# Kernel tuning notes

Hardware: AMD Instinct MI355X
Metric: run time of the kernel (lower is better)

Reference implementation:

```python
import jax, jax.numpy as jnp
import numpy as np

B, S, L, C, H, D, CP = 32, 4, 64, 32, 4, 8, 16  # batch, tracks, bins, c_msa, heads, d_head, c_pair


def _ln(x, g, b, eps=1e-5):
    m = jnp.mean(x, axis=-1, keepdims=True)
    v = jnp.mean((x - m) ** 2, axis=-1, keepdims=True)
    return (x - m) / jnp.sqrt(v + eps) * g + b


def setup_inputs() -> dict:
    key = jax.random.key(0)
    ks = jax.random.split(key, 20)
    n = lambda k, shape, s=0.1: jax.random.normal(k, shape, jnp.float32) * s
    return dict(
        chip_ctcf=n(ks[0], (B, L), 1.0),
        chip_hac=n(ks[1], (B, L), 1.0),
        chip_me1=n(ks[2], (B, L), 1.0),
        chip_me3=n(ks[3], (B, L), 1.0),
        bulk_map=n(ks[4], (B, 1, L, L), 1.0),
        we_w=n(ks[5], (C, 1)), we_b=jnp.zeros((C,), jnp.float32),
        pos=n(ks[6], (1, 1, L, C)),
        mn_g=jnp.ones((C,), jnp.float32), mn_b=jnp.zeros((C,), jnp.float32),
        wq=n(ks[7], (C, C)), bq=jnp.zeros((C,), jnp.float32),
        wk=n(ks[8], (C, C)), bk=jnp.zeros((C,), jnp.float32),
        wv=n(ks[9], (C, C)), bv=jnp.zeros((C,), jnp.float32),
        wo=n(ks[10], (C, C)), bo=jnp.zeros((C,), jnp.float32),
        an_g=jnp.ones((C,), jnp.float32), an_b=jnp.zeros((C,), jnp.float32),
        conv_w=n(ks[11], (H,)), conv_b=jnp.zeros((H,), jnp.float32),
        gate_w=n(ks[12], (H, D, D)), gate_b=jnp.zeros((H, D), jnp.float32),
        pp_w=n(ks[13], (CP, C * C), 0.03), pp_b=jnp.zeros((CP,), jnp.float32),
        ada_g=jnp.ones((CP,), jnp.float32), ada_b=jnp.zeros((CP,), jnp.float32),
        ada_alpha=jnp.ones((1,), jnp.float32),
    )


def reference(chip_ctcf, chip_hac, chip_me1, chip_me3, bulk_map,
              we_w, we_b, pos, mn_g, mn_b,
              wq, bq, wk, bk, wv, bv, wo, bo, an_g, an_b,
              conv_w, conv_b, gate_w, gate_b,
              pp_w, pp_b, ada_g, ada_b, ada_alpha):
    # 1) build MSA: (B, S=4, L, C)
    signals = jnp.stack([chip_ctcf, chip_hac, chip_me1, chip_me3], axis=1)  # (B,S,L)
    msa = signals[..., None] * we_w[:, 0] + we_b                            # Linear(1,C)
    x = _ln(msa + pos, mn_g, mn_b)                                          # (B,S,L,C)

    # 2) row self-attention with bulk-derived per-head bias
    q = (x @ wq.T + bq).reshape(B, S, L, H, D)
    k = (x @ wk.T + bk).reshape(B, S, L, H, D)
    v = (x @ wv.T + bv).reshape(B, S, L, H, D)
    scores = jnp.einsum('bslhd,bsmhd->bshlm', q, k) / jnp.sqrt(jnp.float32(D))
    bias = bulk_map * conv_w.reshape(1, H, 1, 1) + conv_b.reshape(1, H, 1, 1)  # 1x1 conv -> (B,H,L,L)
    attn = jax.nn.softmax(scores + bias[:, None], axis=-1)                     # (B,S,H,L,L)
    out = jnp.einsum('bshlm,bsmhd->bshld', attn, v)
    gate = jax.nn.sigmoid(jnp.einsum('hcd,bshld->bshlc', gate_w, out)
                          + gate_b[None, None, :, None, :])
    out = out * gate
    out = out.transpose(0, 1, 3, 2, 4).reshape(B, S, L, C)
    out = out @ wo.T + bo
    x = _ln(x + out, an_g, an_b)                                            # post-attn LayerNorm

    # 3) outer-product (of max over tracks) pair features
    m = jnp.max(x, axis=1)                                                  # (B,L,C)
    pair = jnp.einsum('bic,bjd->bijcd', m, m).reshape(B, L, L, C * C)       # (B,L,L,1024)
    nrm = jnp.sqrt(jnp.sum(pair * pair, axis=-1, keepdims=True))
    pair = pair / jnp.maximum(nrm, 1e-6)                                    # F.normalize
    feat = pair @ pp_w.T + pp_b                                             # (B,L,L,CP)
    feat = feat + ada_alpha * _ln(feat, ada_g, ada_b)                       # AdaNorm
    feat = jax.nn.silu(feat)
    return feat.transpose(0, 3, 1, 2)                                       # (B,CP,L,L)
```

## Files before the change

### kernel.cpp

```cpp
#include <hip/hip_runtime.h>
#include <hip/hip_bf16.h>

#define NB 32
#define NS 4
#define NL 64
#define NC 32
#define NH 4
#define ND 8
#define NCP 16

using fp = const float* __restrict__;

__global__ __launch_bounds__(256) void k1_attn(
    fp ctcf, fp hac, fp me1, fp me3, fp bulk,
    fp we_w, fp we_b, fp pos, fp mn_g, fp mn_b,
    fp wq, fp bq, fp wk, fp bk, fp wv, fp bv,
    fp wo, fp bo, fp an_g, fp an_b,
    fp conv_w, fp conv_b, fp gate_w, fp gate_b,
    float* __restrict__ xpostT)
{
    __shared__ float ks_s[NC*NL];
    __shared__ float vs_s[NC*NL];
    __shared__ float ao_s[NC*NL];
    __shared__ float bulk_s[NL*65];
    __shared__ float red1[256], red2[256];

    const int t = threadIdx.x;
    const int w = t >> 6;
    const int l = t & 63;
    const int b = blockIdx.x >> 2;
    const int s = blockIdx.x & 3;

    for (int idx = t; idx < NL*NL; idx += 256)
        bulk_s[(idx >> 6)*65 + (idx & 63)] = bulk[b*NL*NL + idx];

    fp sigp = (s == 0) ? ctcf : (s == 1) ? hac : (s == 2) ? me1 : me3;
    const float sig = sigp[b*NL + l];

    float x[NC];
    float mean = 0.f;
#pragma unroll
    for (int c = 0; c < NC; c++){
        x[c] = sig * we_w[c] + we_b[c] + pos[l*NC + c];
        mean += x[c];
    }
    mean *= (1.f/NC);
    float var = 0.f;
#pragma unroll
    for (int c = 0; c < NC; c++){ float d = x[c] - mean; var += d*d; }
    var *= (1.f/NC);
    float inv = rsqrtf(var + 1e-5f);
#pragma unroll
    for (int c = 0; c < NC; c++) x[c] = (x[c] - mean)*inv*mn_g[c] + mn_b[c];

    float q[ND];
#pragma unroll
    for (int e8 = 0; e8 < ND; e8++){
        int e = w*ND + e8;
        float aq = bq[e], ak = bk[e], av = bv[e];
#pragma unroll
        for (int c = 0; c < NC; c++){
            float xv = x[c];
            aq += xv * wq[e*NC + c];
            ak += xv * wk[e*NC + c];
            av += xv * wv[e*NC + c];
        }
        q[e8] = aq;
        ks_s[e*NL + l] = ak;
        vs_s[e*NL + l] = av;
    }
    __syncthreads();

    const float rs8 = 0.35355339059327373f;
    const float cw = conv_w[w], cb = conv_b[w];
    float srow[NL];
    float mx = -1e30f;
    for (int m = 0; m < NL; m++){
        float dot = 0.f;
#pragma unroll
        for (int d = 0; d < ND; d++)
            dot += q[d] * ks_s[(w*ND + d)*NL + m];
        float v = dot*rs8 + bulk_s[l*65 + m]*cw + cb;
        srow[m] = v;
        mx = fmaxf(mx, v);
    }
    float sm = 0.f;
    for (int m = 0; m < NL; m++){ srow[m] = __expf(srow[m] - mx); sm += srow[m]; }
    float is = 1.f / sm;
    float o[ND];
#pragma unroll
    for (int d = 0; d < ND; d++) o[d] = 0.f;
    for (int m = 0; m < NL; m++){
        float a = srow[m] * is;
#pragma unroll
        for (int d = 0; d < ND; d++)
            o[d] += a * vs_s[(w*ND + d)*NL + m];
    }
#pragma unroll
    for (int c8 = 0; c8 < ND; c8++){
        float g = gate_b[w*ND + c8];
#pragma unroll
        for (int d = 0; d < ND; d++) g += gate_w[(w*ND + c8)*ND + d] * o[d];
        ao_s[(w*ND + c8)*NL + l] = o[c8] * (1.f/(1.f + __expf(-g)));
    }
    __syncthreads();

    float p8[ND];
    float psum = 0.f, psq = 0.f;
#pragma unroll
    for (int c8 = 0; c8 < ND; c8++){
        int c = w*ND + c8;
        float a = bo[c];
#pragma unroll
        for (int e = 0; e < NC; e++) a += ao_s[e*NL + l] * wo[c*NC + e];
        float val = x[c] + a;
        p8[c8] = val; psum += val; psq += val*val;
    }
    red1[w*64 + l] = psum;
    red2[w*64 + l] = psq;
    __syncthreads();
    float sum = 0.f, ssq = 0.f;
#pragma unroll
    for (int ww = 0; ww < 4; ww++){ sum += red1[ww*64 + l]; ssq += red2[ww*64 + l]; }
    mean = sum * (1.f/NC);
    var  = ssq * (1.f/NC) - mean*mean;
    inv  = rsqrtf(var + 1e-5f);
#pragma unroll
    for (int c8 = 0; c8 < ND; c8++){
        int c = w*ND + c8;
        xpostT[((b*NS + s)*NC + c)*NL + l] = (p8[c8] - mean)*inv*an_g[c] + an_b[c];
    }
}

__global__ __launch_bounds__(256) void k23_pair(
    const float* __restrict__ xpostT, fp pp_w,
    fp pp_b, fp ada_g, fp ada_b, fp ada_alpha,
    float* __restrict__ out)
{
    __shared__ float ppws[8*NC*NC];
    __shared__ float mh[NC*NL];
    __shared__ float u[NCP*4*NC];

    const int b  = blockIdx.x >> 4;
    const int it = blockIdx.x & 15;
    const int t  = threadIdx.x;
    const int w  = t >> 6;
    const int j  = t & 63;

    const float* xb = xpostT + b*NS*NC*NL;
#pragma unroll
    for (int k = 0; k < 8; k++){
        int cj = k*256 + t;
        float v = xb[cj];
        v = fmaxf(v, xb[NC*NL + cj]);
        v = fmaxf(v, xb[2*NC*NL + cj]);
        v = fmaxf(v, xb[3*NC*NL + cj]);
        mh[cj] = v;
    }
    __syncthreads();

    if (t < NL){
        float sq = 0.f;
#pragma unroll
        for (int c = 0; c < NC; c++){ float v = mh[c*NL + t]; sq += v*v; }
        u[t] = 1.f / fmaxf(sqrtf(sq), 1e-3f);
    }
    {
        const float4* src = (const float4*)(pp_w);
        float4* dst = (float4*)ppws;
#pragma unroll
        for (int k = 0; k < 8; k++) dst[k*256 + t] = src[k*256 + t];
    }
    __syncthreads();

#pragma unroll
    for (int k = 0; k < 8; k++){
        int cj = k*256 + t;
        mh[cj] *= u[cj & 63];
    }
    __syncthreads();

    float md[NC];
#pragma unroll
    for (int c = 0; c < NC; c++) md[c] = mh[c*NL + j];

#pragma unroll
    for (int loop = 0; loop < 4; loop++){
        int idx = loop*256 + t;
        int d  = idx & 31;
        int ip = (idx >> 5) & 3;
        int pl = idx >> 7;
        int i  = it*4 + ip;
        float acc = 0.f;
#pragma unroll
        for (int c = 0; c < NC; c++)
            acc += mh[c*NL + i] * ppws[pl*1024 + c*32 + d];
        u[pl*128 + ip*32 + d] = acc;
    }
    __syncthreads();

    {
        const float4* src = (const float4*)(pp_w + 8*NC*NC);
        float4* dst = (float4*)ppws;
#pragma unroll
        for (int k = 0; k < 8; k++) dst[k*256 + t] = src[k*256 + t];
    }
    __syncthreads();

#pragma unroll
    for (int loop = 0; loop < 4; loop++){
        int idx = loop*256 + t;
        int d  = idx & 31;
        int ip = (idx >> 5) & 3;
        int pl = idx >> 7;
        int i  = it*4 + ip;
        float acc = 0.f;
#pragma unroll
        for (int c = 0; c < NC; c++)
            acc += mh[c*NL + i] * ppws[pl*1024 + c*32 + d];
        u[(8 + pl)*128 + ip*32 + d] = acc;
    }
    __syncthreads();

    float f[NCP];
#pragma unroll 1
    for (int p = 0; p < NCP; p++){
        float a = 0.f;
#pragma unroll
        for (int d = 0; d < NC; d++)
            a += u[p*128 + w*32 + d] * md[d];
        f[p] = a;
    }

    const float alpha = ada_alpha[0];
    float fsum = 0.f, fsq = 0.f;
#pragma unroll
    for (int p = 0; p < NCP; p++){
        float v = f[p] + pp_b[p];
        f[p] = v; fsum += v; fsq += v*v;
    }
    float fmean = fsum * (1.f/NCP);
    float fvar  = fsq * (1.f/NCP) - fmean*fmean;
    float finv  = rsqrtf(fvar + 1e-5f);
    const int i = it*4 + w;
#pragma unroll
    for (int p = 0; p < NCP; p++){
        float v = f[p] + alpha * ((f[p] - fmean)*finv*ada_g[p] + ada_b[p]);
        out[((b*NCP + p)*NL + i)*NL + j] = v / (1.f + __expf(-v));
    }
}

extern "C" void kernel_launch(void* const* d_in, const int* in_sizes, int n_in,
                              void* d_out, int out_size, void* d_ws, size_t ws_size,
                              hipStream_t stream)
{
    float* xpostT = (float*)d_ws;

    k1_attn<<<NB*NS, 256, 0, stream>>>(
        (fp)d_in[0], (fp)d_in[1], (fp)d_in[2], (fp)d_in[3], (fp)d_in[4],
        (fp)d_in[5], (fp)d_in[6], (fp)d_in[7], (fp)d_in[8], (fp)d_in[9],
        (fp)d_in[10], (fp)d_in[11], (fp)d_in[12], (fp)d_in[13], (fp)d_in[14], (fp)d_in[15],
        (fp)d_in[16], (fp)d_in[17], (fp)d_in[18], (fp)d_in[19],
        (fp)d_in[20], (fp)d_in[21], (fp)d_in[22], (fp)d_in[23], xpostT);

    k23_pair<<<NB*16, 256, 0, stream>>>(
        xpostT, (fp)d_in[24], (fp)d_in[25], (fp)d_in[26], (fp)d_in[27], (fp)d_in[28],
        (float*)d_out);
}
```

Before: 143.0 us.

## Split attention kernel into two row-halves with key-split softmax across lane pairs

The attention kernel now launches two blocks per (batch, track), each handling 32 query rows. Within a block, each query row is processed by a pair of lanes, each covering half of the keys, and the max, sum and output are combined with xor shuffles. The intent is to double the grid from 128 to 256 blocks so more of the GPU's compute units are busy, and to shrink each thread's score array to cut register pressure. In exchange, each block recomputes the full Q/K/V projection and LayerNorm for all 64 rows, and the code adds shared-memory staging plus an extra reduction step for the post-attention LayerNorm.

Result: no change. 142.8 us (median of 2 runs) (-0.2%).

```diff
diff --git a/kernel.cpp b/kernel.cpp
--- a/kernel.cpp
+++ b/kernel.cpp
@@ -19,20 +19,27 @@
     fp conv_w, fp conv_b, fp gate_w, fp gate_b,
     float* __restrict__ xpostT)
 {
+    __shared__ float qs_s[NC*NL];
     __shared__ float ks_s[NC*NL];
     __shared__ float vs_s[NC*NL];
+    __shared__ float xs_s[NC*NL];
     __shared__ float ao_s[NC*NL];
-    __shared__ float bulk_s[NL*65];
-    __shared__ float red1[256], red2[256];
-
-    const int t = threadIdx.x;
-    const int w = t >> 6;
-    const int l = t & 63;
-    const int b = blockIdx.x >> 2;
-    const int s = blockIdx.x & 3;
-
-    for (int idx = t; idx < NL*NL; idx += 256)
-        bulk_s[(idx >> 6)*65 + (idx & 63)] = bulk[b*NL*NL + idx];
+    __shared__ float bulk_s[32*65];
+    __shared__ float red1[32*8], red2[32*8];
+    __shared__ float mstat[32], istat[32];
+
+    const int t    = threadIdx.x;
+    const int w    = t >> 6;
+    const int l    = t & 63;
+    const int bx   = blockIdx.x;
+    const int b    = bx >> 3;
+    const int s    = (bx >> 1) & 3;
+    const int half = bx & 1;
+
+    for (int idx = t; idx < 32*NL; idx += 256){
+        int lr = idx >> 6, m = idx & 63;
+        bulk_s[lr*65 + m] = bulk[b*NL*NL + (half*32 + lr)*NL + m];
+    }
 
     fp sigp = (s == 0) ? ctcf : (s == 1) ? hac : (s == 2) ? me1 : me3;
     const float sig = sigp[b*NL + l];
@@ -53,7 +60,6 @@
 #pragma unroll
     for (int c = 0; c < NC; c++) x[c] = (x[c] - mean)*inv*mn_g[c] + mn_b[c];
 
-    float q[ND];
 #pragma unroll
     for (int e8 = 0; e8 < ND; e8++){
         int e = w*ND + e8;
@@ -65,70 +71,98 @@
             ak += xv * wk[e*NC + c];
             av += xv * wv[e*NC + c];
         }
-        q[e8] = aq;
+        qs_s[e*NL + l] = aq;
         ks_s[e*NL + l] = ak;
         vs_s[e*NL + l] = av;
-    }
-    __syncthreads();
+        xs_s[e*NL + l] = x[e];
+    }
+    __syncthreads();
+
+    const int rl  = l >> 1;
+    const int r   = half*32 + rl;
+    const int mh_ = l & 1;
+    const int m0  = mh_*32;
+
+    float q8[ND];
+#pragma unroll
+    for (int d = 0; d < ND; d++) q8[d] = qs_s[(w*ND + d)*NL + r];
 
     const float rs8 = 0.35355339059327373f;
     const float cw = conv_w[w], cb = conv_b[w];
-    float srow[NL];
+    float srow[32];
     float mx = -1e30f;
-    for (int m = 0; m < NL; m++){
+    for (int mi = 0; mi < 32; mi++){
+        int m = m0 + mi;
         float dot = 0.f;
 #pragma unroll
         for (int d = 0; d < ND; d++)
-            dot += q[d] * ks_s[(w*ND + d)*NL + m];
-        float v = dot*rs8 + bulk_s[l*65 + m]*cw + cb;
-        srow[m] = v;
+            dot += q8[d] * ks_s[(w*ND + d)*NL + m];
+        float v = dot*rs8 + bulk_s[rl*65 + m]*cw + cb;
+        srow[mi] = v;
         mx = fmaxf(mx, v);
     }
+    mx = fmaxf(mx, __shfl_xor(mx, 1));
     float sm = 0.f;
-    for (int m = 0; m < NL; m++){ srow[m] = __expf(srow[m] - mx); sm += srow[m]; }
+    for (int mi = 0; mi < 32; mi++){ srow[mi] = __expf(srow[mi] - mx); sm += srow[mi]; }
+    sm += __shfl_xor(sm, 1);
     float is = 1.f / sm;
+
     float o[ND];
 #pragma unroll
     for (int d = 0; d < ND; d++) o[d] = 0.f;
-    for (int m = 0; m < NL; m++){
-        float a = srow[m] * is;
+    for (int mi = 0; mi < 32; mi++){
+        float a = srow[mi] * is;
 #pragma unroll
         for (int d = 0; d < ND; d++)
-            o[d] += a * vs_s[(w*ND + d)*NL + m];
-    }
-#pragma unroll
-    for (int c8 = 0; c8 < ND; c8++){
+            o[d] += a * vs_s[(w*ND + d)*NL + m0 + mi];
+    }
+#pragma unroll
+    for (int d = 0; d < ND; d++) o[d] += __shfl_xor(o[d], 1);
+
+#pragma unroll
+    for (int k = 0; k < 4; k++){
+        int c8 = mh_*4 + k;
         float g = gate_b[w*ND + c8];
 #pragma unroll
         for (int d = 0; d < ND; d++) g += gate_w[(w*ND + c8)*ND + d] * o[d];
-        ao_s[(w*ND + c8)*NL + l] = o[c8] * (1.f/(1.f + __expf(-g)));
-    }
-    __syncthreads();
-
-    float p8[ND];
+        ao_s[(w*ND + c8)*NL + r] = o[c8] * (1.f/(1.f + __expf(-g)));
+    }
+    __syncthreads();
+
+    const int r3  = t & 31;
+    const int rg  = half*32 + r3;
+    const int cg  = t >> 5;
+    float vals[4];
     float psum = 0.f, psq = 0.f;
 #pragma unroll
-    for (int c8 = 0; c8 < ND; c8++){
-        int c = w*ND + c8;
+    for (int k = 0; k < 4; k++){
+        int c = cg*4 + k;
         float a = bo[c];
 #pragma unroll
-        for (int e = 0; e < NC; e++) a += ao_s[e*NL + l] * wo[c*NC + e];
-        float val = x[c] + a;
-        p8[c8] = val; psum += val; psq += val*val;
-    }
-    red1[w*64 + l] = psum;
-    red2[w*64 + l] = psq;
-    __syncthreads();
-    float sum = 0.f, ssq = 0.f;
-#pragma unroll
-    for (int ww = 0; ww < 4; ww++){ sum += red1[ww*64 + l]; ssq += red2[ww*64 + l]; }
-    mean = sum * (1.f/NC);
-    var  = ssq * (1.f/NC) - mean*mean;
-    inv  = rsqrtf(var + 1e-5f);
-#pragma unroll
-    for (int c8 = 0; c8 < ND; c8++){
-        int c = w*ND + c8;
-        xpostT[((b*NS + s)*NC + c)*NL + l] = (p8[c8] - mean)*inv*an_g[c] + an_b[c];
+        for (int e = 0; e < NC; e++) a += ao_s[e*NL + rg] * wo[c*NC + e];
+        float val = xs_s[c*NL + rg] + a;
+        vals[k] = val; psum += val; psq += val*val;
+    }
+    red1[r3*8 + cg] = psum;
+    red2[r3*8 + cg] = psq;
+    __syncthreads();
+    if (t < 32){
+        float sum = 0.f, ssq = 0.f;
+#pragma unroll
+        for (int g = 0; g < 8; g++){ sum += red1[t*8 + g]; ssq += red2[t*8 + g]; }
+        float mn = sum * (1.f/NC);
+        float vr = ssq * (1.f/NC) - mn*mn;
+        mstat[t] = mn;
+        istat[t] = rsqrtf(vr + 1e-5f);
+    }
+    __syncthreads();
+    {
+        float mn = mstat[r3], iv = istat[r3];
+#pragma unroll
+        for (int k = 0; k < 4; k++){
+            int c = cg*4 + k;
+            xpostT[((b*NS + s)*NC + c)*NL + rg] = (vals[k] - mn)*iv*an_g[c] + an_b[c];
+        }
     }
 }
 
@@ -256,7 +290,7 @@
 {
     float* xpostT = (float*)d_ws;
 
-    k1_attn<<<NB*NS, 256, 0, stream>>>(
+    k1_attn<<<NB*NS*2, 256, 0, stream>>>(
         (fp)d_in[0], (fp)d_in[1], (fp)d_in[2], (fp)d_in[3], (fp)d_in[4],
         (fp)d_in[5], (fp)d_in[6], (fp)d_in[7], (fp)d_in[8], (fp)d_in[9],
         (fp)d_in[10], (fp)d_in[11], (fp)d_in[12], (fp)d_in[13], (fp)d_in[14], (fp)d_in[15],
```

## Fuse attention and pair-feature kernels into one kernel with recomputed attention

Applied to the files above, without the earlier changes.

Merges the two kernels into a single launch: each block handles one batch and an 8-row slab of output, and recomputes all four tracks' attention (one wave per track, each thread doing all heads) instead of reading a workspace tensor. This removes the intermediate global round-trip and a launch boundary, and swaps the padded bulk tile for an XOR-swizzled layout. In exchange, attention work is duplicated 8x across blocks, per-thread register pressure rises sharply (q[32], ao[32], x[32]), and the grid shrinks to 256 blocks.

Measured after the change: 247.8 us. 1.73x slower.

```diff
diff --git a/kernel.cpp b/kernel.cpp
--- a/kernel.cpp
+++ b/kernel.cpp
@@ -11,32 +11,34 @@
 
 using fp = const float* __restrict__;
 
-__global__ __launch_bounds__(256) void k1_attn(
+__global__ __launch_bounds__(256, 2) void kall(
     fp ctcf, fp hac, fp me1, fp me3, fp bulk,
     fp we_w, fp we_b, fp pos, fp mn_g, fp mn_b,
     fp wq, fp bq, fp wk, fp bk, fp wv, fp bv,
     fp wo, fp bo, fp an_g, fp an_b,
     fp conv_w, fp conv_b, fp gate_w, fp gate_b,
-    float* __restrict__ xpostT)
+    fp pp_w, fp pp_b, fp ada_g, fp ada_b, fp ada_alpha,
+    float* __restrict__ out)
 {
-    __shared__ float ks_s[NC*NL];
-    __shared__ float vs_s[NC*NL];
-    __shared__ float ao_s[NC*NL];
-    __shared__ float bulk_s[NL*65];
-    __shared__ float red1[256], red2[256];
-
-    const int t = threadIdx.x;
-    const int w = t >> 6;
-    const int l = t & 63;
-    const int b = blockIdx.x >> 2;
-    const int s = blockIdx.x & 3;
-
-    for (int idx = t; idx < NL*NL; idx += 256)
-        bulk_s[(idx >> 6)*65 + (idx & 63)] = bulk[b*NL*NL + idx];
-
-    fp sigp = (s == 0) ? ctcf : (s == 1) ? hac : (s == 2) ? me1 : me3;
+    __shared__ float A[8192];
+    __shared__ float V[8192];
+    __shared__ float bulk_s[4096];
+
+    const int t  = threadIdx.x;
+    const int w  = t >> 6;
+    const int l  = t & 63;
+    const int b  = blockIdx.x >> 3;
+    const int it = blockIdx.x & 7;
+
+#pragma unroll
+    for (int k = 0; k < 16; k++){
+        int idx = k*256 + t;
+        int row = idx >> 6, col = idx & 63;
+        bulk_s[row*64 + (col ^ (row & 31))] = bulk[b*4096 + idx];
+    }
+
+    fp sigp = (w == 0) ? ctcf : (w == 1) ? hac : (w == 2) ? me1 : me3;
     const float sig = sigp[b*NL + l];
-
     float x[NC];
     float mean = 0.f;
 #pragma unroll
@@ -53,10 +55,9 @@
 #pragma unroll
     for (int c = 0; c < NC; c++) x[c] = (x[c] - mean)*inv*mn_g[c] + mn_b[c];
 
-    float q[ND];
-#pragma unroll
-    for (int e8 = 0; e8 < ND; e8++){
-        int e = w*ND + e8;
+    float q[NC];
+#pragma unroll
+    for (int e = 0; e < NC; e++){
         float aq = bq[e], ak = bk[e], av = bv[e];
 #pragma unroll
         for (int c = 0; c < NC; c++){
@@ -65,109 +66,99 @@
             ak += xv * wk[e*NC + c];
             av += xv * wv[e*NC + c];
         }
-        q[e8] = aq;
-        ks_s[e*NL + l] = ak;
-        vs_s[e*NL + l] = av;
+        q[e] = aq;
+        A[w*2048 + e*64 + l] = ak;
+        V[w*2048 + e*64 + l] = av;
     }
     __syncthreads();
 
     const float rs8 = 0.35355339059327373f;
-    const float cw = conv_w[w], cb = conv_b[w];
-    float srow[NL];
-    float mx = -1e30f;
-    for (int m = 0; m < NL; m++){
-        float dot = 0.f;
-#pragma unroll
-        for (int d = 0; d < ND; d++)
-            dot += q[d] * ks_s[(w*ND + d)*NL + m];
-        float v = dot*rs8 + bulk_s[l*65 + m]*cw + cb;
-        srow[m] = v;
-        mx = fmaxf(mx, v);
-    }
-    float sm = 0.f;
-    for (int m = 0; m < NL; m++){ srow[m] = __expf(srow[m] - mx); sm += srow[m]; }
-    float is = 1.f / sm;
-    float o[ND];
-#pragma unroll
-    for (int d = 0; d < ND; d++) o[d] = 0.f;
-    for (int m = 0; m < NL; m++){
-        float a = srow[m] * is;
-#pragma unroll
-        for (int d = 0; d < ND; d++)
-            o[d] += a * vs_s[(w*ND + d)*NL + m];
-    }
-#pragma unroll
-    for (int c8 = 0; c8 < ND; c8++){
-        float g = gate_b[w*ND + c8];
-#pragma unroll
-        for (int d = 0; d < ND; d++) g += gate_w[(w*ND + c8)*ND + d] * o[d];
-        ao_s[(w*ND + c8)*NL + l] = o[c8] * (1.f/(1.f + __expf(-g)));
-    }
-    __syncthreads();
-
-    float p8[ND];
-    float psum = 0.f, psq = 0.f;
-#pragma unroll
-    for (int c8 = 0; c8 < ND; c8++){
-        int c = w*ND + c8;
-        float a = bo[c];
-#pragma unroll
-        for (int e = 0; e < NC; e++) a += ao_s[e*NL + l] * wo[c*NC + e];
-        float val = x[c] + a;
-        p8[c8] = val; psum += val; psq += val*val;
-    }
-    red1[w*64 + l] = psum;
-    red2[w*64 + l] = psq;
-    __syncthreads();
-    float sum = 0.f, ssq = 0.f;
-#pragma unroll
-    for (int ww = 0; ww < 4; ww++){ sum += red1[ww*64 + l]; ssq += red2[ww*64 + l]; }
-    mean = sum * (1.f/NC);
-    var  = ssq * (1.f/NC) - mean*mean;
-    inv  = rsqrtf(var + 1e-5f);
-#pragma unroll
-    for (int c8 = 0; c8 < ND; c8++){
-        int c = w*ND + c8;
-        xpostT[((b*NS + s)*NC + c)*NL + l] = (p8[c8] - mean)*inv*an_g[c] + an_b[c];
-    }
-}
-
-__global__ __launch_bounds__(256) void k23_pair(
-    const float* __restrict__ xpostT, fp pp_w,
-    fp pp_b, fp ada_g, fp ada_b, fp ada_alpha,
-    float* __restrict__ out)
-{
-    __shared__ float ppws[8*NC*NC];
-    __shared__ float mh[NC*NL];
-    __shared__ float u[NCP*4*NC];
-
-    const int b  = blockIdx.x >> 4;
-    const int it = blockIdx.x & 15;
-    const int t  = threadIdx.x;
-    const int w  = t >> 6;
-    const int j  = t & 63;
-
-    const float* xb = xpostT + b*NS*NC*NL;
-#pragma unroll
-    for (int k = 0; k < 8; k++){
-        int cj = k*256 + t;
-        float v = xb[cj];
-        v = fmaxf(v, xb[NC*NL + cj]);
-        v = fmaxf(v, xb[2*NC*NL + cj]);
-        v = fmaxf(v, xb[3*NC*NL + cj]);
-        mh[cj] = v;
-    }
-    __syncthreads();
-
+    float ao[NC];
+    for (int h = 0; h < NH; h++){
+        const float cw = conv_w[h], cb = conv_b[h];
+        float srow[NL];
+        float mx = -1e30f;
+        for (int m = 0; m < NL; m++){
+            float dot = 0.f;
+#pragma unroll
+            for (int d = 0; d < ND; d++)
+                dot += q[h*ND + d] * A[w*2048 + (h*ND + d)*64 + m];
+            float v = dot*rs8 + bulk_s[l*64 + (m ^ (l & 31))]*cw + cb;
+            srow[m] = v;
+            mx = fmaxf(mx, v);
+        }
+        float sm = 0.f;
+        for (int m = 0; m < NL; m++){ srow[m] = __expf(srow[m] - mx); sm += srow[m]; }
+        float is = 1.f / sm;
+        float o[ND];
+#pragma unroll
+        for (int d = 0; d < ND; d++) o[d] = 0.f;
+        for (int m = 0; m < NL; m++){
+            float a = srow[m] * is;
+#pragma unroll
+            for (int d = 0; d < ND; d++)
+                o[d] += a * V[w*2048 + (h*ND + d)*64 + m];
+        }
+#pragma unroll
+        for (int c8 = 0; c8 < ND; c8++){
+            float g = gate_b[h*ND + c8];
+#pragma unroll
+            for (int d = 0; d < ND; d++) g += gate_w[(h*ND + c8)*ND + d] * o[d];
+            ao[h*ND + c8] = o[c8] * (1.f/(1.f + __expf(-g)));
+        }
+    }
+    __syncthreads();
+
+    {
+        float xp[NC];
+        float mn2 = 0.f;
+#pragma unroll
+        for (int c = 0; c < NC; c++){
+            float a = bo[c];
+#pragma unroll
+            for (int e = 0; e < NC; e++) a += ao[e] * wo[c*NC + e];
+            float val = x[c] + a;
+            xp[c] = val; mn2 += val;
+        }
+        mn2 *= (1.f/NC);
+        float vr = 0.f;
+#pragma unroll
+        for (int c = 0; c < NC; c++){ float d = xp[c] - mn2; vr += d*d; }
+        vr *= (1.f/NC);
+        float iv = rsqrtf(vr + 1e-5f);
+#pragma unroll
+        for (int c = 0; c < NC; c++)
+            A[w*2048 + c*64 + l] = (xp[c] - mn2)*iv*an_g[c] + an_b[c];
+    }
+    __syncthreads();
+
+#pragma unroll
+    for (int k = 0; k < 8; k++){
+        int cl = k*256 + t;
+        float v = A[cl];
+        v = fmaxf(v, A[2048 + cl]);
+        v = fmaxf(v, A[4096 + cl]);
+        v = fmaxf(v, A[6144 + cl]);
+        V[cl] = v;
+    }
+    __syncthreads();
     if (t < NL){
         float sq = 0.f;
 #pragma unroll
-        for (int c = 0; c < NC; c++){ float v = mh[c*NL + t]; sq += v*v; }
-        u[t] = 1.f / fmaxf(sqrtf(sq), 1e-3f);
-    }
+        for (int c = 0; c < NC; c++){ float v = V[c*64 + t]; sq += v*v; }
+        V[6144 + t] = 1.f / fmaxf(sqrtf(sq), 1e-3f);
+    }
+    __syncthreads();
+#pragma unroll
+    for (int k = 0; k < 8; k++){
+        int cl = k*256 + t;
+        V[cl] *= V[6144 + (cl & 63)];
+    }
+    __syncthreads();
+
     {
         const float4* src = (const float4*)(pp_w);
-        float4* dst = (float4*)ppws;
+        float4* dst = (float4*)A;
 #pragma unroll
         for (int k = 0; k < 8; k++) dst[k*256 + t] = src[k*256 + t];
     }
@@ -175,78 +166,69 @@
 
 #pragma unroll
     for (int k = 0; k < 8; k++){
-        int cj = k*256 + t;
-        mh[cj] *= u[cj & 63];
-    }
-    __syncthreads();
-
-    float md[NC];
-#pragma unroll
-    for (int c = 0; c < NC; c++) md[c] = mh[c*NL + j];
-
-#pragma unroll
-    for (int loop = 0; loop < 4; loop++){
-        int idx = loop*256 + t;
+        int idx = k*256 + t;
         int d  = idx & 31;
-        int ip = (idx >> 5) & 3;
-        int pl = idx >> 7;
-        int i  = it*4 + ip;
+        int ip = (idx >> 5) & 7;
+        int pl = idx >> 8;
         float acc = 0.f;
 #pragma unroll
         for (int c = 0; c < NC; c++)
-            acc += mh[c*NL + i] * ppws[pl*1024 + c*32 + d];
-        u[pl*128 + ip*32 + d] = acc;
+            acc += V[c*64 + it*8 + ip] * A[pl*1024 + c*32 + d];
+        V[2048 + pl*256 + ip*32 + d] = acc;
     }
     __syncthreads();
 
     {
         const float4* src = (const float4*)(pp_w + 8*NC*NC);
-        float4* dst = (float4*)ppws;
+        float4* dst = (float4*)A;
 #pragma unroll
         for (int k = 0; k < 8; k++) dst[k*256 + t] = src[k*256 + t];
     }
     __syncthreads();
 
 #pragma unroll
-    for (int loop = 0; loop < 4; loop++){
-        int idx = loop*256 + t;
+    for (int k = 0; k < 8; k++){
+        int idx = k*256 + t;
         int d  = idx & 31;
-        int ip = (idx >> 5) & 3;
-        int pl = idx >> 7;
-        int i  = it*4 + ip;
+        int ip = (idx >> 5) & 7;
+        int pl = idx >> 8;
         float acc = 0.f;
 #pragma unroll
         for (int c = 0; c < NC; c++)
-            acc += mh[c*NL + i] * ppws[pl*1024 + c*32 + d];
-        u[(8 + pl)*128 + ip*32 + d] = acc;
-    }
-    __syncthreads();
-
-    float f[NCP];
-#pragma unroll 1
-    for (int p = 0; p < NCP; p++){
-        float a = 0.f;
-#pragma unroll
-        for (int d = 0; d < NC; d++)
-            a += u[p*128 + w*32 + d] * md[d];
-        f[p] = a;
-    }
+            acc += V[c*64 + it*8 + ip] * A[pl*1024 + c*32 + d];
+        V[4096 + pl*256 + ip*32 + d] = acc;
+    }
+    __syncthreads();
+
+    const int j = l;
+    float md[NC];
+#pragma unroll
+    for (int c = 0; c < NC; c++) md[c] = V[c*64 + j];
 
     const float alpha = ada_alpha[0];
-    float fsum = 0.f, fsq = 0.f;
-#pragma unroll
-    for (int p = 0; p < NCP; p++){
-        float v = f[p] + pp_b[p];
-        f[p] = v; fsum += v; fsq += v*v;
-    }
-    float fmean = fsum * (1.f/NCP);
-    float fvar  = fsq * (1.f/NCP) - fmean*fmean;
-    float finv  = rsqrtf(fvar + 1e-5f);
-    const int i = it*4 + w;
-#pragma unroll
-    for (int p = 0; p < NCP; p++){
-        float v = f[p] + alpha * ((f[p] - fmean)*finv*ada_g[p] + ada_b[p]);
-        out[((b*NCP + p)*NL + i)*NL + j] = v / (1.f + __expf(-v));
+#pragma unroll
+    for (int rep = 0; rep < 2; rep++){
+        const int ip = w + 4*rep;
+        const int i  = it*8 + ip;
+        float f[NCP];
+        float fsum = 0.f, fsq = 0.f;
+#pragma unroll
+        for (int p = 0; p < NCP; p++){
+            float a = 0.f;
+#pragma unroll
+            for (int d = 0; d < NC; d++)
+                a += V[2048 + p*256 + ip*32 + d] * md[d];
+            a += pp_b[p];
+            f[p] = a; fsum += a; fsq += a*a;
+        }
+        float fmean = fsum * (1.f/NCP);
+        float fvar  = fsq * (1.f/NCP) - fmean*fmean;
+        float finv  = rsqrtf(fvar + 1e-5f);
+#pragma unroll
+        for (int p = 0; p < NCP; p++){
+            float v = f[p] + alpha * ((f[p] - fmean)*finv*ada_g[p] + ada_b[p]);
+            out[((b*NCP + p)*NL + i)*NL + j] = v / (1.f + __expf(-v));
+        }
     }
 }
 
@@ -254,16 +236,12 @@
                               void* d_out, int out_size, void* d_ws, size_t ws_size,
                               hipStream_t stream)
 {
-    float* xpostT = (float*)d_ws;
-
-    k1_attn<<<NB*NS, 256, 0, stream>>>(
+    kall<<<NB*8, 256, 0, stream>>>(
         (fp)d_in[0], (fp)d_in[1], (fp)d_in[2], (fp)d_in[3], (fp)d_in[4],
         (fp)d_in[5], (fp)d_in[6], (fp)d_in[7], (fp)d_in[8], (fp)d_in[9],
         (fp)d_in[10], (fp)d_in[11], (fp)d_in[12], (fp)d_in[13], (fp)d_in[14], (fp)d_in[15],
         (fp)d_in[16], (fp)d_in[17], (fp)d_in[18], (fp)d_in[19],
-        (fp)d_in[20], (fp)d_in[21], (fp)d_in[22], (fp)d_in[23], xpostT);
-
-    k23_pair<<<NB*16, 256, 0, stream>>>(
-        xpostT, (fp)d_in[24], (fp)d_in[25], (fp)d_in[26], (fp)d_in[27], (fp)d_in[28],
+        (fp)d_in[20], (fp)d_in[21], (fp)d_in[22], (fp)d_in[23],
+        (fp)d_in[24], (fp)d_in[25], (fp)d_in[26], (fp)d_in[27], (fp)d_in[28],
         (float*)d_out);
 }
```
